# Kernel tuning notes

Hardware: AMD Instinct MI355X
Metric: run time of the kernel (lower is better)

The kernel has to match this reference:

```python
import jax, jax.numpy as jnp
import numpy as np

N = 384          # residues / nodes
E = 12288        # edges (avg degree 32)
D_LM = 1024      # BERT hidden
D_NODE = 256     # extra node features -> D_LM + D_NODE = 1280
D = 1280         # node_emb_size
H = D // 10      # 128, dis/mask MLP hidden
M = 64           # masked positions


def setup_inputs() -> dict:
    key = jax.random.key(0)
    ks = jax.random.split(key, 16)
    s = lambda d_in: 1.0 / np.sqrt(d_in)
    inp = {
        "lm_embedding": jax.random.normal(ks[0], (1, N + 2, D_LM), jnp.float32),
        "node_feat": jax.random.normal(ks[1], (N, D_NODE), jnp.float32),
        # positive distances in [0.5, 1.5) so edge_weight = 1/(d^2+1e-6) is well scaled
        "edge_feat": jax.random.uniform(ks[2], (E, 1), jnp.float32) + 0.5,
        "src": jax.random.randint(ks[3], (E,), 0, N, jnp.int32),
        "dst": jax.random.randint(ks[4], (E,), 0, N, jnp.int32),
        "mask_index": jax.random.randint(ks[5], (M,), 0, N, jnp.int32),
        # GINConv apply-func linears (stored as [in, out]; torch Linear is x @ W.T + b)
        "W_gin0": jax.random.normal(ks[6], (D, D), jnp.float32) * s(D),
        "b_gin0": jnp.zeros((D,), jnp.float32),
        "W_gin1": jax.random.normal(ks[7], (D, D), jnp.float32) * s(D),
        "b_gin1": jnp.zeros((D,), jnp.float32),
        # dis_nn: Linear(D,H) -> ReLU -> Linear(H,30)
        "Wd1": jax.random.normal(ks[8], (D, H), jnp.float32) * s(D),
        "bd1": jnp.zeros((H,), jnp.float32),
        "Wd2": jax.random.normal(ks[9], (H, 30), jnp.float32) * s(H),
        "bd2": jnp.zeros((30,), jnp.float32),
        # mask_nn: Linear(D,H) -> ReLU -> Linear(H,2) -> Tanh
        "Wm1": jax.random.normal(ks[10], (D, H), jnp.float32) * s(D),
        "bm1": jnp.zeros((H,), jnp.float32),
        "Wm2": jax.random.normal(ks[11], (H, 2), jnp.float32) * s(H),
        "bm2": jnp.zeros((2,), jnp.float32),
    }
    return inp


def _gin(x, src, dst, edge_weight, W, b):
    # DGL GINConv (eps=0, 'sum'): Linear( x + sum_{e:(u->v)} w_e * x_u )
    msg = x[src] * edge_weight                      # [E, D] gather-multiply
    agg = jax.ops.segment_sum(msg, dst, num_segments=N)  # scatter-sum to dst
    return (x + agg) @ W + b


def reference(lm_embedding, node_feat, edge_feat, src, dst, mask_index,
              W_gin0, b_gin0, W_gin1, b_gin1,
              Wd1, bd1, Wd2, bd2, Wm1, bm1, Wm2, bm2):
    # node_feat0: strip CLS/SEP tokens, concat with node features -> [N, D]
    node_feat0 = jnp.concatenate([lm_embedding[0, 1:-1, :], node_feat], axis=1)
    edge_weight = 1.0 / (edge_feat ** 2 + 1e-6)     # [E, 1]

    # original uses node_feat0.data (detached) as GIN input
    x0 = jax.lax.stop_gradient(node_feat0)
    h = _gin(x0, src, dst, edge_weight, W_gin0, b_gin0)
    node_output = _gin(h, src, dst, edge_weight, W_gin1, b_gin1)
    node_output = node_output + node_feat0          # residual (use_lm=1)

    # pairwise squared differences: [N, N, D]
    dis_hid = (node_output[None, :, :] - node_output[:, None, :]) ** 2
    dh = dis_hid.reshape(-1, D)                     # [N*N, D]
    dis_pred = jax.nn.relu(dh @ Wd1 + bd1) @ Wd2 + bd2  # [N*N, 30]

    xm = node_output[mask_index]                    # [M, D]
    mask_pred = jnp.tanh(jax.nn.relu(xm @ Wm1 + bm1) @ Wm2 + bm2)  # [M, 2]
    return dis_pred, mask_pred
```

## Files before the change

### kernel.cpp

```cpp
#include <hip/hip_runtime.h>
#include <hip/hip_bf16.h>

#define NN 384
#define EE 12288
#define DD 1280
#define HH 128
#define DISROWS (NN*NN)

typedef short bf16x8 __attribute__((ext_vector_type(8)));
typedef short bf16x4 __attribute__((ext_vector_type(4)));
typedef float f32x4  __attribute__((ext_vector_type(4)));

__device__ __forceinline__ unsigned short f2bf(float x){
  unsigned u = __builtin_bit_cast(unsigned, x);
  u += 0x7fffu + ((u >> 16) & 1u);
  return (unsigned short)(u >> 16);
}
__device__ __forceinline__ float bf2f(unsigned short h){
  unsigned u = ((unsigned)h) << 16;
  return __builtin_bit_cast(float, u);
}
__device__ __forceinline__ short f2bf_fast(float x){
  return (short)__bfloat16_as_ushort(__float2bfloat16(x));
}
__device__ __forceinline__ void glds16(const short* g, short* l){
  __builtin_amdgcn_global_load_lds((const __attribute__((address_space(1))) void*)g,
                                   (__attribute__((address_space(3))) void*)l, 16, 0, 0);
}

__device__ __forceinline__ void tsplit_body(const float* __restrict__ W,
                                            short* __restrict__ Thi, short* __restrict__ Tlo,
                                            int R, int C, int bx, int by, int t,
                                            float* tile ){
  int rb = by*64, cb = bx*64;
  int r  = t >> 2;
  int cs = (t & 3) * 16;
  const float* sp = W + (long)(rb + r)*C + cb + cs;
  #pragma unroll
  for (int i = 0; i < 16; i += 4){
    f32x4 v = *(const f32x4*)(sp + i);
    tile[r*65 + cs+i+0] = v[0]; tile[r*65 + cs+i+1] = v[1];
    tile[r*65 + cs+i+2] = v[2]; tile[r*65 + cs+i+3] = v[3];
  }
  __syncthreads();
  int cp = t >> 2;
  int rs = (t & 3) * 16;
  bf16x8 vh0, vh1, vl0, vl1;
  #pragma unroll
  for (int i = 0; i < 8; ++i){
    float f = tile[(rs+i)*65 + cp];
    unsigned short h = f2bf(f);
    vh0[i] = (short)h; vl0[i] = (short)f2bf(f - bf2f(h));
  }
  #pragma unroll
  for (int i = 0; i < 8; ++i){
    float f = tile[(rs+8+i)*65 + cp];
    unsigned short h = f2bf(f);
    vh1[i] = (short)h; vl1[i] = (short)f2bf(f - bf2f(h));
  }
  long ob = (long)(cb + cp)*R + rb + rs;
  *(bf16x8*)&Thi[ob]   = vh0;
  *(bf16x8*)&Thi[ob+8] = vh1;
  if (Tlo){
    *(bf16x8*)&Tlo[ob]   = vl0;
    *(bf16x8*)&Tlo[ob+8] = vl1;
  }
}

__global__ void k_prep(const float* __restrict__ lm, const float* __restrict__ nf,
                       float* __restrict__ x0,
                       const int* __restrict__ dst, const float* __restrict__ ef,
                       int* __restrict__ offs, int* __restrict__ sorted,
                       float* __restrict__ ew,
                       const float* __restrict__ Wd1, short* __restrict__ W1t,
                       const float* __restrict__ Wd2, short* __restrict__ W2t,
                       const float* __restrict__ Wg0, short* __restrict__ WtAh,
                       short* __restrict__ WtAl){
  __shared__ __align__(16) float sh[64*65];
  const int b = blockIdx.x;
  const int t = threadIdx.x;
  if (b < 960){
    int i = b*512 + t;
    int n = i / 1280;
    int d = i - n*1280;
    x0[i] = (d < 1024) ? lm[(n+1)*1024 + d] : nf[n*256 + (d-1024)];
    return;
  }
  if (b == 960){
    int* cnt = (int*)sh;
    int* base = cnt + 512;
    if (t < 512) cnt[t] = 0;
    __syncthreads();
    for (int e = t; e < EE; e += 512){
      atomicAdd(&cnt[dst[e]], 1);
      float f = ef[e];
      ew[e] = 1.0f/(f*f + 1e-6f);
    }
    __syncthreads();
    for (int off = 1; off < 512; off <<= 1){
      int v = (t >= off) ? cnt[t - off] : 0;
      __syncthreads();
      cnt[t] += v;
      __syncthreads();
    }
    if (t < NN){
      int excl = t ? cnt[t-1] : 0;
      offs[t] = excl;
      base[t] = excl;
    }
    if (t == 0) offs[NN] = EE;
    __syncthreads();
    for (int e = t; e < EE; e += 512){
      int p = atomicAdd(&base[dst[e]], 1);
      sorted[p] = e;
    }
    return;
  }
  if (b < 1002){
    int g = b - 961;
    if (g < 40){
      if (t < 256) tsplit_body(Wd1, W1t, nullptr, DD, HH, g & 1, g >> 1, t, sh);
      else { __syncthreads(); }
      return;
    }
    for (int i = t; i < 32*HH; i += 512){
      int c = i >> 7, h = i & 127;
      float v = (c < 30) ? Wd2[h*30 + c] : 0.f;
      W2t[i] = (short)f2bf(v);
    }
    return;
  }
  {
    int g = b - 1002;
    if (t < 256) tsplit_body(Wg0, WtAh, WtAl, DD, DD, g % 20, g / 20, t, sh);
    else { __syncthreads(); }
  }
}

__global__ void k_agg(const float* __restrict__ X, const float* __restrict__ ew,
                      const int* __restrict__ src, const int* __restrict__ offs,
                      const int* __restrict__ sorted,
                      short* __restrict__ Yh, short* __restrict__ Yl){
  __shared__ int   s_off[160];
  __shared__ float s_w[160];
  const int v = blockIdx.x;
  const int d = blockIdx.y*256 + threadIdx.x;
  const int t = threadIdx.x;
  float acc = X[(long)v*DD + d];
  const int b = offs[v], e = offs[v+1];
  for (int c0 = b; c0 < e; c0 += 160){
    int n = e - c0; if (n > 160) n = 160;
    __syncthreads();
    if (t < n){
      int eid = sorted[c0 + t];
      s_off[t] = src[eid]*DD;
      s_w[t]   = ew[eid];
    }
    __syncthreads();
    int k = 0;
    for (; k + 4 <= n; k += 4){
      acc += s_w[k]  *X[s_off[k]   + d];
      acc += s_w[k+1]*X[s_off[k+1] + d];
      acc += s_w[k+2]*X[s_off[k+2] + d];
      acc += s_w[k+3]*X[s_off[k+3] + d];
    }
    for (; k < n; ++k) acc += s_w[k]*X[s_off[k] + d];
  }
  unsigned short h = f2bf(acc);
  Yh[(long)v*DD + d] = (short)h;
  Yl[(long)v*DD + d] = (short)f2bf(acc - bf2f(h));
}

__launch_bounds__(256, 2)
__global__ void k_gin_gemm(const short* __restrict__ Yh, const short* __restrict__ Yl,
                           const short* __restrict__ Whi, const short* __restrict__ Wlo,
                           float* __restrict__ P){
  __shared__ __align__(16) short Ahi[128*40], Alo[128*40], Bhi[128*40], Blo[128*40];
  const int m0 = blockIdx.x*128;
  const int n0 = blockIdx.y*128;
  const int kbase = blockIdx.z*160;
  const int t = threadIdx.x, w = t >> 6, lane = t & 63;
  const int l15 = lane & 15, l4 = lane >> 4;
  f32x4 acc[2][8];
  #pragma unroll
  for (int m = 0; m < 2; ++m)
    #pragma unroll
    for (int n = 0; n < 8; ++n) acc[m][n] = (f32x4){0.f,0.f,0.f,0.f};

  const int row = t >> 1, half = t & 1;
  const short* aph = Yh  + (long)(m0+row)*DD + half*16;
  const short* apl = Yl  + (long)(m0+row)*DD + half*16;
  const short* bph = Whi + (long)(n0+row)*DD + half*16;
  const short* bpl = Wlo + (long)(n0+row)*DD + half*16;

  for (int kk = 0; kk < 5; ++kk){
    int d0 = kbase + kk*32;
    __syncthreads();
    *(bf16x8*)&Ahi[row*40 + half*16]     = *(const bf16x8*)(aph + d0);
    *(bf16x8*)&Ahi[row*40 + half*16 + 8] = *(const bf16x8*)(aph + d0 + 8);
    *(bf16x8*)&Alo[row*40 + half*16]     = *(const bf16x8*)(apl + d0);
    *(bf16x8*)&Alo[row*40 + half*16 + 8] = *(const bf16x8*)(apl + d0 + 8);
    *(bf16x8*)&Bhi[row*40 + half*16]     = *(const bf16x8*)(bph + d0);
    *(bf16x8*)&Bhi[row*40 + half*16 + 8] = *(const bf16x8*)(bph + d0 + 8);
    *(bf16x8*)&Blo[row*40 + half*16]     = *(const bf16x8*)(bpl + d0);
    *(bf16x8*)&Blo[row*40 + half*16 + 8] = *(const bf16x8*)(bpl + d0 + 8);
    __syncthreads();

    bf16x8 ah[2], al[2];
    #pragma unroll
    for (int m = 0; m < 2; ++m){
      int rr = w*32 + m*16 + l15;
      ah[m] = *(const bf16x8*)&Ahi[rr*40 + l4*8];
      al[m] = *(const bf16x8*)&Alo[rr*40 + l4*8];
    }
    #pragma unroll
    for (int n = 0; n < 8; ++n){
      int rr = n*16 + l15;
      bf16x8 bh = *(const bf16x8*)&Bhi[rr*40 + l4*8];
      bf16x8 bl = *(const bf16x8*)&Blo[rr*40 + l4*8];
      #pragma unroll
      for (int m = 0; m < 2; ++m){
        acc[m][n] = __builtin_amdgcn_mfma_f32_16x16x32_bf16(ah[m], bh, acc[m][n], 0,0,0);
        acc[m][n] = __builtin_amdgcn_mfma_f32_16x16x32_bf16(ah[m], bl, acc[m][n], 0,0,0);
        acc[m][n] = __builtin_amdgcn_mfma_f32_16x16x32_bf16(al[m], bh, acc[m][n], 0,0,0);
      }
    }
  }
  float* Pz = P + (long)blockIdx.z*NN*DD;
  #pragma unroll
  for (int m = 0; m < 2; ++m){
    #pragma unroll
    for (int n = 0; n < 8; ++n){
      int gr0 = m0 + w*32 + m*16 + l4*4;
      int gc  = n0 + n*16 + l15;
      #pragma unroll
      for (int r = 0; r < 4; ++r)
        Pz[(long)(gr0+r)*DD + gc] = acc[m][n][r];
    }
  }
}

__global__ void k_red_t(const float* __restrict__ P, const float* __restrict__ bias,
                        const float* __restrict__ resid, float* __restrict__ Out,
                        const float* __restrict__ Wg1, short* __restrict__ WtAh,
                        short* __restrict__ WtAl){
  __shared__ __align__(16) float sh[64*65];
  const int b = blockIdx.x;
  if (b >= 480){
    if (Wg1){
      int g = b - 480;
      tsplit_body(Wg1, WtAh, WtAl, DD, DD, g % 20, g / 20, threadIdx.x, sh);
    }
    return;
  }
  const int i = b*256 + threadIdx.x;
  const int col = (i*4) % DD;
  const f32x4* P4 = (const f32x4*)P;
  f32x4 s = P4[i];
  #pragma unroll
  for (int z = 1; z < 8; ++z) s += P4[i + z*122880];
  s += *(const f32x4*)(bias + col);
  if (resid) s += ((const f32x4*)resid)[i];
  ((f32x4*)Out)[i] = s;
}

__launch_bounds__(256, 3)
__global__ void k_dis(const float* __restrict__ X, const short* __restrict__ W1t,
                      const float* __restrict__ bd1, const short* __restrict__ W2t,
                      const float* __restrict__ bd2, float* __restrict__ out,
                      const int* __restrict__ midx,
                      const float* __restrict__ Wm1, const float* __restrict__ bm1,
                      const float* __restrict__ Wm2, const float* __restrict__ bm2){
  __shared__ __align__(16) short smem[25088];
  const int b = blockIdx.x;
  const int t = threadIdx.x;

  if (b >= 600){
    float* tl = (float*)smem;
    int m = b - 600;
    if (t < HH){
      const float* x = X + (long)midx[m]*DD;
      float a0 = 0.f, a1 = 0.f, a2 = 0.f, a3 = 0.f;
      for (int d = 0; d < DD; d += 4){
        a0 += x[d]   * Wm1[(d)*HH + t];
        a1 += x[d+1] * Wm1[(d+1)*HH + t];
        a2 += x[d+2] * Wm1[(d+2)*HH + t];
        a3 += x[d+3] * Wm1[(d+3)*HH + t];
      }
      float v = a0 + a1 + a2 + a3 + bm1[t];
      tl[t] = v > 0.f ? v : 0.f;
    }
    __syncthreads();
    if (t < 2){
      float s = bm2[t];
      for (int h = 0; h < HH; ++h) s += tl[h]*Wm2[h*2 + t];
      out[(long)DISROWS*30 + m*2 + t] = tanhf(s);
    }
    return;
  }

  int k = 0, rem = b;
  while (rem >= 2*(24 - k)){ rem -= 2*(24 - k); ++k; }
  int ib = 2*k;
  if (rem >= 24 - k){ ++ib; rem -= 24 - k; }
  const int jb = k + rem;
  const int i0 = ib*8, j0 = jb*16;

  const int w = t >> 6, lane = t & 63;
  const int l15 = lane & 15, l4 = lane >> 4;

  short* WA = smem;
  float* XF = (float*)(smem + 16384);
  short* TL = smem;
  float* OT = (float*)(smem + 17408);

  f32x4 acc[2][8];
  #pragma unroll
  for (int m = 0; m < 2; ++m)
    #pragma unroll
    for (int n = 0; n < 8; ++n) acc[m][n] = (f32x4){0.f,0.f,0.f,0.f};

  const short* wsrc[4];
  #pragma unroll
  for (int i = 0; i < 4; ++i){
    int hb = w*32 + i*8 + (lane >> 3);
    wsrc[i] = W1t + (long)hb*DD + (((lane & 7) ^ (hb & 7))*8);
  }
  const float* xsrc[6];
  int xli[6];
  #pragma unroll
  for (int g = 0; g < 6; ++g){
    int idx = g*256 + t;
    int rowl = idx >> 6, col = idx & 63;
    int grow = (rowl < 8) ? (i0 + rowl) : (j0 + rowl - 8);
    xsrc[g] = X + (long)grow*DD + col;
    xli[g] = rowl*68 + col;
  }

  float xr[6];
  #pragma unroll
  for (int i = 0; i < 4; ++i)
    glds16(wsrc[i], WA + (w*32 + i*8)*64);
  #pragma unroll
  for (int g = 0; g < 6; ++g) xr[g] = xsrc[g][0];
  #pragma unroll
  for (int g = 0; g < 6; ++g) XF[xli[g]] = xr[g];
  __syncthreads();

  for (int mk = 0; mk < 20; ++mk){
    const int cb = mk & 1;
    short* WAc = WA + cb*8192;
    float* XFc = XF + cb*1632;
    short* WAn = WA + (cb^1)*8192;
    float* XFn = XF + (cb^1)*1632;
    if (mk < 19){
      #pragma unroll
      for (int i = 0; i < 4; ++i)
        glds16(wsrc[i] + (mk+1)*64, WAn + (w*32 + i*8)*64);
      #pragma unroll
      for (int g = 0; g < 6; ++g) xr[g] = xsrc[g][(mk+1)*64];
    }
    #pragma unroll
    for (int ks = 0; ks < 2; ++ks){
      f32x4 xj0 = *(const f32x4*)&XFc[(8 + l15)*68 + ks*32 + l4*8];
      f32x4 xj1 = *(const f32x4*)&XFc[(8 + l15)*68 + ks*32 + l4*8 + 4];
      bf16x8 a[2];
      #pragma unroll
      for (int m = 0; m < 2; ++m){
        const float* xip = &XFc[(2*w + m)*68 + ks*32 + l4*8];
        f32x4 xi0 = *(const f32x4*)xip;
        f32x4 xi1 = *(const f32x4*)(xip + 4);
        f32x4 d0 = xj0 - xi0; d0 = d0*d0;
        f32x4 d1 = xj1 - xi1; d1 = d1*d1;
        bf16x8 av;
        #pragma unroll
        for (int q = 0; q < 4; ++q){
          av[q]   = f2bf_fast(d0[q]);
          av[4+q] = f2bf_fast(d1[q]);
        }
        a[m] = av;
      }
      #pragma unroll
      for (int n = 0; n < 8; ++n){
        bf16x8 wf = *(const bf16x8*)&WAc[(n*16 + l15)*64 + (((ks*4 + l4) ^ (l15 & 7))*8)];
        acc[0][n] = __builtin_amdgcn_mfma_f32_16x16x32_bf16(wf, a[0], acc[0][n], 0,0,0);
        acc[1][n] = __builtin_amdgcn_mfma_f32_16x16x32_bf16(wf, a[1], acc[1][n], 0,0,0);
      }
    }
    if (mk < 19){
      #pragma unroll
      for (int g = 0; g < 6; ++g) XFn[xli[g]] = xr[g];
    }
    __syncthreads();
  }

  f32x4 bd1v[8];
  #pragma unroll
  for (int n = 0; n < 8; ++n) bd1v[n] = *(const f32x4*)(bd1 + n*16 + l4*4);
  #pragma unroll
  for (int m = 0; m < 2; ++m){
    int pair = (2*w + m)*16 + l15;
    #pragma unroll
    for (int n = 0; n < 8; ++n){
      bf16x4 pv;
      #pragma unroll
      for (int r = 0; r < 4; ++r){
        float v = acc[m][n][r] + bd1v[n][r];
        v = v > 0.f ? v : 0.f;
        pv[r] = f2bf_fast(v);
      }
      *(bf16x4*)&TL[pair*136 + n*16 + l4*4] = pv;
    }
  }
  __syncthreads();

  f32x4 acc2[2][2];
  #pragma unroll
  for (int m2 = 0; m2 < 2; ++m2)
    #pragma unroll
    for (int nn = 0; nn < 2; ++nn) acc2[m2][nn] = (f32x4){0.f,0.f,0.f,0.f};
  #pragma unroll
  for (int hs = 0; hs < 4; ++hs){
    bf16x8 b2[2];
    #pragma unroll
    for (int nn = 0; nn < 2; ++nn)
      b2[nn] = *(const bf16x8*)&W2t[(nn*16 + l15)*HH + hs*32 + l4*8];
    #pragma unroll
    for (int m2 = 0; m2 < 2; ++m2){
      bf16x8 a2 = *(const bf16x8*)&TL[(w*32 + m2*16 + l15)*136 + hs*32 + l4*8];
      #pragma unroll
      for (int nn = 0; nn < 2; ++nn)
        acc2[m2][nn] = __builtin_amdgcn_mfma_f32_16x16x32_bf16(a2, b2[nn], acc2[m2][nn], 0,0,0);
    }
  }
  #pragma unroll
  for (int m2 = 0; m2 < 2; ++m2){
    #pragma unroll
    for (int nn = 0; nn < 2; ++nn){
      int cc = nn*16 + l15;
      if (cc < 30){
        float b2v = bd2[cc];
        #pragma unroll
        for (int r = 0; r < 4; ++r)
          OT[(w*32 + m2*16 + l4*4 + r)*30 + cc] = acc2[m2][nn][r] + b2v;
      }
    }
  }
  __syncthreads();

  {
    int i = t >> 5;
    int ca = (t & 31)*15;
    long nbase = ((long)(i0 + i)*NN + j0)*30 + ca;
    const float* nsrc = OT + i*480 + ca;
    #pragma unroll
    for (int q = 0; q < 15; ++q) out[nbase + q] = nsrc[q];
    int j = t >> 4;
    int s = t & 15;
    int ii = s >> 1;
    int c0 = (s & 1)*15;
    long mbase = ((long)(j0 + j)*NN + i0 + ii)*30 + c0;
    const float* msrc = OT + ii*480 + j*30 + c0;
    #pragma unroll
    for (int q = 0; q < 15; ++q) out[mbase + q] = msrc[q];
  }
}

extern "C" void kernel_launch(void* const* d_in, const int* in_sizes, int n_in,
                              void* d_out, int out_size, void* d_ws, size_t ws_size,
                              hipStream_t stream){
  const float* lm   = (const float*)d_in[0];
  const float* nf   = (const float*)d_in[1];
  const float* ef   = (const float*)d_in[2];
  const int*   src  = (const int*)d_in[3];
  const int*   dst  = (const int*)d_in[4];
  const int*   midx = (const int*)d_in[5];
  const float* Wg0  = (const float*)d_in[6];
  const float* bg0  = (const float*)d_in[7];
  const float* Wg1  = (const float*)d_in[8];
  const float* bg1  = (const float*)d_in[9];
  const float* Wd1  = (const float*)d_in[10];
  const float* bd1  = (const float*)d_in[11];
  const float* Wd2  = (const float*)d_in[12];
  const float* bd2  = (const float*)d_in[13];
  const float* Wm1  = (const float*)d_in[14];
  const float* bm1  = (const float*)d_in[15];
  const float* Wm2  = (const float*)d_in[16];
  const float* bm2  = (const float*)d_in[17];
  float* dis = (float*)d_out;

  char* ws = (char*)d_ws;
  size_t off = 0;
  auto alloc = [&](size_t bytes)->void*{
    void* p = ws + off; off += (bytes + 255) & ~(size_t)255; return p;
  };
  float* x0   = (float*)alloc((size_t)NN*DD*4);
  float* hb   = (float*)alloc((size_t)NN*DD*4);
  short* Yh   = (short*)alloc((size_t)NN*DD*2);
  short* Yl   = (short*)alloc((size_t)NN*DD*2);
  float* ew   = (float*)alloc((size_t)EE*4);
  int*   offs = (int*)alloc((NN+1)*4);
  int*   sorted = (int*)alloc(EE*4);
  short* WtAh = (short*)alloc((size_t)DD*DD*2);
  short* WtAl = (short*)alloc((size_t)DD*DD*2);
  short* W1t  = (short*)alloc((size_t)HH*DD*2);
  short* W2t  = (short*)alloc((size_t)32*HH*2);
  float* P    = (float*)alloc((size_t)8*NN*DD*4);

  k_prep<<<1402,512,0,stream>>>(lm, nf, x0, dst, ef, offs, sorted, ew,
                                Wd1, W1t, Wd2, W2t, Wg0, WtAh, WtAl);

  k_agg<<<dim3(384,5),256,0,stream>>>(x0, ew, src, offs, sorted, Yh, Yl);
  k_gin_gemm<<<dim3(3,10,8),256,0,stream>>>(Yh, Yl, WtAh, WtAl, P);
  k_red_t<<<880,256,0,stream>>>(P, bg0, nullptr, hb, Wg1, WtAh, WtAl);

  k_agg<<<dim3(384,5),256,0,stream>>>(hb, ew, src, offs, sorted, Yh, Yl);
  k_gin_gemm<<<dim3(3,10,8),256,0,stream>>>(Yh, Yl, WtAh, WtAl, P);
  k_red_t<<<480,256,0,stream>>>(P, bg1, x0, hb, nullptr, nullptr, nullptr);

  k_dis<<<664,256,0,stream>>>(hb, W1t, bd1, W2t, bd2, dis,
                              midx, Wm1, bm1, Wm2, bm2);
}
```

Before: 121.5 us.

## Drop x0 materialization, pretranspose both GIN weights in prep, halve GEMM M-tile

Removes the concatenated x0 buffer: the first aggregation reads lm/node_feat directly and the final reduction adds the residual from the original inputs. Both GIN weight matrices are now transposed and split in the prep kernel into separate buffers, so the reduction kernel no longer carries transpose blocks. The GIN GEMM uses 64-row M tiles with one MFMA row-block per wave and occupancy 4, doubling the grid to fill more CUs. The costs are extra branching in k_agg, a larger workspace for the second weight copy, and less B-tile reuse per block.

```diff
diff --git a/kernel.cpp b/kernel.cpp
--- a/kernel.cpp
+++ b/kernel.cpp
@@ -67,26 +67,19 @@
   }
 }
 
-__global__ void k_prep(const float* __restrict__ lm, const float* __restrict__ nf,
-                       float* __restrict__ x0,
-                       const int* __restrict__ dst, const float* __restrict__ ef,
+__global__ void k_prep(const int* __restrict__ dst, const float* __restrict__ ef,
                        int* __restrict__ offs, int* __restrict__ sorted,
                        float* __restrict__ ew,
                        const float* __restrict__ Wd1, short* __restrict__ W1t,
                        const float* __restrict__ Wd2, short* __restrict__ W2t,
                        const float* __restrict__ Wg0, short* __restrict__ WtAh,
-                       short* __restrict__ WtAl){
+                       short* __restrict__ WtAl,
+                       const float* __restrict__ Wg1, short* __restrict__ WtBh,
+                       short* __restrict__ WtBl){
   __shared__ __align__(16) float sh[64*65];
   const int b = blockIdx.x;
   const int t = threadIdx.x;
-  if (b < 960){
-    int i = b*512 + t;
-    int n = i / 1280;
-    int d = i - n*1280;
-    x0[i] = (d < 1024) ? lm[(n+1)*1024 + d] : nf[n*256 + (d-1024)];
-    return;
-  }
-  if (b == 960){
+  if (b == 0){
     int* cnt = (int*)sh;
     int* base = cnt + 512;
     if (t < 512) cnt[t] = 0;
@@ -116,8 +109,8 @@
     }
     return;
   }
-  if (b < 1002){
-    int g = b - 961;
+  if (b < 42){
+    int g = b - 1;
     if (g < 40){
       if (t < 256) tsplit_body(Wd1, W1t, nullptr, DD, HH, g & 1, g >> 1, t, sh);
       else { __syncthreads(); }
@@ -130,137 +123,147 @@
     }
     return;
   }
-  {
-    int g = b - 1002;
+  if (b < 442){
+    int g = b - 42;
     if (t < 256) tsplit_body(Wg0, WtAh, WtAl, DD, DD, g % 20, g / 20, t, sh);
     else { __syncthreads(); }
-  }
-}
-
-__global__ void k_agg(const float* __restrict__ X, const float* __restrict__ ew,
-                      const int* __restrict__ src, const int* __restrict__ offs,
-                      const int* __restrict__ sorted,
+    return;
+  }
+  {
+    int g = b - 442;
+    if (t < 256) tsplit_body(Wg1, WtBh, WtBl, DD, DD, g % 20, g / 20, t, sh);
+    else { __syncthreads(); }
+  }
+}
+
+__global__ void k_agg(const float* __restrict__ X,
+                      const float* __restrict__ lm, const float* __restrict__ nf,
+                      const float* __restrict__ ew, const int* __restrict__ src,
+                      const int* __restrict__ offs, const int* __restrict__ sorted,
                       short* __restrict__ Yh, short* __restrict__ Yl){
-  __shared__ int   s_off[160];
+  __shared__ int   s_nd[160];
   __shared__ float s_w[160];
   const int v = blockIdx.x;
-  const int d = blockIdx.y*256 + threadIdx.x;
+  const int y = blockIdx.y;
   const int t = threadIdx.x;
-  float acc = X[(long)v*DD + d];
+  const int d = y*256 + t;
+  float acc;
+  if (X)           acc = X[(long)v*DD + d];
+  else if (y < 4)  acc = lm[(long)(v+1)*1024 + d];
+  else             acc = nf[(long)v*256 + t];
   const int b = offs[v], e = offs[v+1];
   for (int c0 = b; c0 < e; c0 += 160){
     int n = e - c0; if (n > 160) n = 160;
     __syncthreads();
     if (t < n){
       int eid = sorted[c0 + t];
-      s_off[t] = src[eid]*DD;
-      s_w[t]   = ew[eid];
-    }
-    __syncthreads();
-    int k = 0;
-    for (; k + 4 <= n; k += 4){
-      acc += s_w[k]  *X[s_off[k]   + d];
-      acc += s_w[k+1]*X[s_off[k+1] + d];
-      acc += s_w[k+2]*X[s_off[k+2] + d];
-      acc += s_w[k+3]*X[s_off[k+3] + d];
-    }
-    for (; k < n; ++k) acc += s_w[k]*X[s_off[k] + d];
+      s_nd[t] = src[eid];
+      s_w[t]  = ew[eid];
+    }
+    __syncthreads();
+    if (X){
+      int k = 0;
+      for (; k + 4 <= n; k += 4){
+        acc += s_w[k]  *X[(long)s_nd[k]*DD + d];
+        acc += s_w[k+1]*X[(long)s_nd[k+1]*DD + d];
+        acc += s_w[k+2]*X[(long)s_nd[k+2]*DD + d];
+        acc += s_w[k+3]*X[(long)s_nd[k+3]*DD + d];
+      }
+      for (; k < n; ++k) acc += s_w[k]*X[(long)s_nd[k]*DD + d];
+    } else if (y < 4){
+      int k = 0;
+      for (; k + 4 <= n; k += 4){
+        acc += s_w[k]  *lm[(long)(s_nd[k]+1)*1024 + d];
+        acc += s_w[k+1]*lm[(long)(s_nd[k+1]+1)*1024 + d];
+        acc += s_w[k+2]*lm[(long)(s_nd[k+2]+1)*1024 + d];
+        acc += s_w[k+3]*lm[(long)(s_nd[k+3]+1)*1024 + d];
+      }
+      for (; k < n; ++k) acc += s_w[k]*lm[(long)(s_nd[k]+1)*1024 + d];
+    } else {
+      int k = 0;
+      for (; k + 4 <= n; k += 4){
+        acc += s_w[k]  *nf[(long)s_nd[k]*256 + t];
+        acc += s_w[k+1]*nf[(long)s_nd[k+1]*256 + t];
+        acc += s_w[k+2]*nf[(long)s_nd[k+2]*256 + t];
+        acc += s_w[k+3]*nf[(long)s_nd[k+3]*256 + t];
+      }
+      for (; k < n; ++k) acc += s_w[k]*nf[(long)s_nd[k]*256 + t];
+    }
   }
   unsigned short h = f2bf(acc);
   Yh[(long)v*DD + d] = (short)h;
   Yl[(long)v*DD + d] = (short)f2bf(acc - bf2f(h));
 }
 
-__launch_bounds__(256, 2)
+__launch_bounds__(256, 4)
 __global__ void k_gin_gemm(const short* __restrict__ Yh, const short* __restrict__ Yl,
                            const short* __restrict__ Whi, const short* __restrict__ Wlo,
                            float* __restrict__ P){
-  __shared__ __align__(16) short Ahi[128*40], Alo[128*40], Bhi[128*40], Blo[128*40];
-  const int m0 = blockIdx.x*128;
+  __shared__ __align__(16) short Ahi[64*40], Alo[64*40], Bhi[128*40], Blo[128*40];
+  const int m0 = blockIdx.x*64;
   const int n0 = blockIdx.y*128;
   const int kbase = blockIdx.z*160;
   const int t = threadIdx.x, w = t >> 6, lane = t & 63;
   const int l15 = lane & 15, l4 = lane >> 4;
-  f32x4 acc[2][8];
-  #pragma unroll
-  for (int m = 0; m < 2; ++m)
-    #pragma unroll
-    for (int n = 0; n < 8; ++n) acc[m][n] = (f32x4){0.f,0.f,0.f,0.f};
-
-  const int row = t >> 1, half = t & 1;
-  const short* aph = Yh  + (long)(m0+row)*DD + half*16;
-  const short* apl = Yl  + (long)(m0+row)*DD + half*16;
-  const short* bph = Whi + (long)(n0+row)*DD + half*16;
-  const short* bpl = Wlo + (long)(n0+row)*DD + half*16;
+  f32x4 acc[8];
+  #pragma unroll
+  for (int n = 0; n < 8; ++n) acc[n] = (f32x4){0.f,0.f,0.f,0.f};
+
+  const int arow = t >> 2, aq = t & 3;
+  const short* aph = Yh  + (long)(m0+arow)*DD + aq*8;
+  const short* apl = Yl  + (long)(m0+arow)*DD + aq*8;
+  const int brow = t >> 1, bh2 = t & 1;
+  const short* bph = Whi + (long)(n0+brow)*DD + bh2*16;
+  const short* bpl = Wlo + (long)(n0+brow)*DD + bh2*16;
 
   for (int kk = 0; kk < 5; ++kk){
     int d0 = kbase + kk*32;
     __syncthreads();
-    *(bf16x8*)&Ahi[row*40 + half*16]     = *(const bf16x8*)(aph + d0);
-    *(bf16x8*)&Ahi[row*40 + half*16 + 8] = *(const bf16x8*)(aph + d0 + 8);
-    *(bf16x8*)&Alo[row*40 + half*16]     = *(const bf16x8*)(apl + d0);
-    *(bf16x8*)&Alo[row*40 + half*16 + 8] = *(const bf16x8*)(apl + d0 + 8);
-    *(bf16x8*)&Bhi[row*40 + half*16]     = *(const bf16x8*)(bph + d0);
-    *(bf16x8*)&Bhi[row*40 + half*16 + 8] = *(const bf16x8*)(bph + d0 + 8);
-    *(bf16x8*)&Blo[row*40 + half*16]     = *(const bf16x8*)(bpl + d0);
-    *(bf16x8*)&Blo[row*40 + half*16 + 8] = *(const bf16x8*)(bpl + d0 + 8);
-    __syncthreads();
-
-    bf16x8 ah[2], al[2];
-    #pragma unroll
-    for (int m = 0; m < 2; ++m){
-      int rr = w*32 + m*16 + l15;
-      ah[m] = *(const bf16x8*)&Ahi[rr*40 + l4*8];
-      al[m] = *(const bf16x8*)&Alo[rr*40 + l4*8];
-    }
+    *(bf16x8*)&Ahi[arow*40 + aq*8] = *(const bf16x8*)(aph + d0);
+    *(bf16x8*)&Alo[arow*40 + aq*8] = *(const bf16x8*)(apl + d0);
+    *(bf16x8*)&Bhi[brow*40 + bh2*16]     = *(const bf16x8*)(bph + d0);
+    *(bf16x8*)&Bhi[brow*40 + bh2*16 + 8] = *(const bf16x8*)(bph + d0 + 8);
+    *(bf16x8*)&Blo[brow*40 + bh2*16]     = *(const bf16x8*)(bpl + d0);
+    *(bf16x8*)&Blo[brow*40 + bh2*16 + 8] = *(const bf16x8*)(bpl + d0 + 8);
+    __syncthreads();
+
+    bf16x8 ah = *(const bf16x8*)&Ahi[(w*16 + l15)*40 + l4*8];
+    bf16x8 al = *(const bf16x8*)&Alo[(w*16 + l15)*40 + l4*8];
     #pragma unroll
     for (int n = 0; n < 8; ++n){
-      int rr = n*16 + l15;
-      bf16x8 bh = *(const bf16x8*)&Bhi[rr*40 + l4*8];
-      bf16x8 bl = *(const bf16x8*)&Blo[rr*40 + l4*8];
-      #pragma unroll
-      for (int m = 0; m < 2; ++m){
-        acc[m][n] = __builtin_amdgcn_mfma_f32_16x16x32_bf16(ah[m], bh, acc[m][n], 0,0,0);
-        acc[m][n] = __builtin_amdgcn_mfma_f32_16x16x32_bf16(ah[m], bl, acc[m][n], 0,0,0);
-        acc[m][n] = __builtin_amdgcn_mfma_f32_16x16x32_bf16(al[m], bh, acc[m][n], 0,0,0);
-      }
+      bf16x8 bh = *(const bf16x8*)&Bhi[(n*16 + l15)*40 + l4*8];
+      bf16x8 bl = *(const bf16x8*)&Blo[(n*16 + l15)*40 + l4*8];
+      acc[n] = __builtin_amdgcn_mfma_f32_16x16x32_bf16(ah, bh, acc[n], 0,0,0);
+      acc[n] = __builtin_amdgcn_mfma_f32_16x16x32_bf16(ah, bl, acc[n], 0,0,0);
+      acc[n] = __builtin_amdgcn_mfma_f32_16x16x32_bf16(al, bh, acc[n], 0,0,0);
     }
   }
   float* Pz = P + (long)blockIdx.z*NN*DD;
   #pragma unroll
-  for (int m = 0; m < 2; ++m){
-    #pragma unroll
-    for (int n = 0; n < 8; ++n){
-      int gr0 = m0 + w*32 + m*16 + l4*4;
-      int gc  = n0 + n*16 + l15;
-      #pragma unroll
-      for (int r = 0; r < 4; ++r)
-        Pz[(long)(gr0+r)*DD + gc] = acc[m][n][r];
-    }
-  }
-}
-
-__global__ void k_red_t(const float* __restrict__ P, const float* __restrict__ bias,
-                        const float* __restrict__ resid, float* __restrict__ Out,
-                        const float* __restrict__ Wg1, short* __restrict__ WtAh,
-                        short* __restrict__ WtAl){
-  __shared__ __align__(16) float sh[64*65];
-  const int b = blockIdx.x;
-  if (b >= 480){
-    if (Wg1){
-      int g = b - 480;
-      tsplit_body(Wg1, WtAh, WtAl, DD, DD, g % 20, g / 20, threadIdx.x, sh);
-    }
-    return;
-  }
-  const int i = b*256 + threadIdx.x;
+  for (int n = 0; n < 8; ++n){
+    int gc = n0 + n*16 + l15;
+    #pragma unroll
+    for (int r = 0; r < 4; ++r)
+      Pz[(long)(m0 + w*16 + l4*4 + r)*DD + gc] = acc[n][r];
+  }
+}
+
+__global__ void k_red(const float* __restrict__ P, const float* __restrict__ bias,
+                      const float* __restrict__ lm, const float* __restrict__ nf,
+                      float* __restrict__ Out){
+  const int i = blockIdx.x*256 + threadIdx.x;
   const int col = (i*4) % DD;
+  const int row = (i*4) / DD;
   const f32x4* P4 = (const f32x4*)P;
   f32x4 s = P4[i];
   #pragma unroll
   for (int z = 1; z < 8; ++z) s += P4[i + z*122880];
   s += *(const f32x4*)(bias + col);
-  if (resid) s += ((const f32x4*)resid)[i];
+  if (lm){
+    f32x4 r = (col < 1024) ? *(const f32x4*)(lm + (long)(row+1)*1024 + col)
+                           : *(const f32x4*)(nf + (long)row*256 + col - 1024);
+    s += r;
+  }
   ((f32x4*)Out)[i] = s;
 }
 
@@ -494,7 +497,7 @@
   auto alloc = [&](size_t bytes)->void*{
     void* p = ws + off; off += (bytes + 255) & ~(size_t)255; return p;
   };
-  float* x0   = (float*)alloc((size_t)NN*DD*4);
+  float* hb0  = (float*)alloc((size_t)NN*DD*4);
   float* hb   = (float*)alloc((size_t)NN*DD*4);
   short* Yh   = (short*)alloc((size_t)NN*DD*2);
   short* Yl   = (short*)alloc((size_t)NN*DD*2);
@@ -503,20 +506,23 @@
   int*   sorted = (int*)alloc(EE*4);
   short* WtAh = (short*)alloc((size_t)DD*DD*2);
   short* WtAl = (short*)alloc((size_t)DD*DD*2);
+  short* WtBh = (short*)alloc((size_t)DD*DD*2);
+  short* WtBl = (short*)alloc((size_t)DD*DD*2);
   short* W1t  = (short*)alloc((size_t)HH*DD*2);
   short* W2t  = (short*)alloc((size_t)32*HH*2);
   float* P    = (float*)alloc((size_t)8*NN*DD*4);
 
-  k_prep<<<1402,512,0,stream>>>(lm, nf, x0, dst, ef, offs, sorted, ew,
-                                Wd1, W1t, Wd2, W2t, Wg0, WtAh, WtAl);
-
-  k_agg<<<dim3(384,5),256,0,stream>>>(x0, ew, src, offs, sorted, Yh, Yl);
-  k_gin_gemm<<<dim3(3,10,8),256,0,stream>>>(Yh, Yl, WtAh, WtAl, P);
-  k_red_t<<<880,256,0,stream>>>(P, bg0, nullptr, hb, Wg1, WtAh, WtAl);
-
-  k_agg<<<dim3(384,5),256,0,stream>>>(hb, ew, src, offs, sorted, Yh, Yl);
-  k_gin_gemm<<<dim3(3,10,8),256,0,stream>>>(Yh, Yl, WtAh, WtAl, P);
-  k_red_t<<<480,256,0,stream>>>(P, bg1, x0, hb, nullptr, nullptr, nullptr);
+  k_prep<<<842,512,0,stream>>>(dst, ef, offs, sorted, ew,
+                               Wd1, W1t, Wd2, W2t,
+                               Wg0, WtAh, WtAl, Wg1, WtBh, WtBl);
+
+  k_agg<<<dim3(384,5),256,0,stream>>>(nullptr, lm, nf, ew, src, offs, sorted, Yh, Yl);
+  k_gin_gemm<<<dim3(6,10,8),256,0,stream>>>(Yh, Yl, WtAh, WtAl, P);
+  k_red<<<480,256,0,stream>>>(P, bg0, nullptr, nullptr, hb0);
+
+  k_agg<<<dim3(384,5),256,0,stream>>>(hb0, lm, nf, ew, src, offs, sorted, Yh, Yl);
+  k_gin_gemm<<<dim3(6,10,8),256,0,stream>>>(Yh, Yl, WtBh, WtBl, P);
+  k_red<<<480,256,0,stream>>>(P, bg1, lm, nf, hb);
 
   k_dis<<<664,256,0,stream>>>(hb, W1t, bd1, W2t, bd2, dis,
                               midx, Wm1, bm1, Wm2, bm2);
```

After: 123.2 us. About the same (+1.4%).
